# Kernel optimization log

Measured on AMD Instinct MI355X. Metric: run time of the kernel, lower is better.

The kernel has to match this reference:

```python
import jax, jax.numpy as jnp
import numpy as np


def setup_inputs() -> dict:
    key = jax.random.key(0)
    ks = jax.random.split(key, 7)
    B, N, Fin, Fout = 32, 1024, 64, 64
    s = 1.0 / np.sqrt(Fin)
    return {
        "X": jax.random.normal(ks[0], (B, N, Fin), dtype=jnp.float32),
        "A": jax.random.normal(ks[1], (B, N, N), dtype=jnp.float32),  # unused in forward, kept for signature fidelity
        "W": jax.random.uniform(ks[2], (Fin, Fout), jnp.float32, -s, s),
        "att_W": jax.random.uniform(ks[3], (Fin, Fout), jnp.float32, -s, s),
        "a": jax.random.uniform(ks[4], (Fout, Fout), jnp.float32, -s, s),
        "bias_W": jax.random.uniform(ks[5], (Fout,), jnp.float32, -s, s),
        "self_W": jax.random.uniform(ks[6], (Fin, Fout), jnp.float32, -s, s),
    }


def reference(X, A, W, att_W, a, bias_W, self_W):
    # att_X = X @ att_W : [B, N, Fout]
    att_X = jnp.einsum('bnf,fg->bng', X, att_W)
    # torch einsum 'ij,ajk->ajk' sums `a` over i => per-feature scale a.sum(0)
    scale = jnp.sum(a, axis=0)  # [Fout]
    # Z[b,i,k] = sum_j att_X[b,i,j] * scale[j] * att_X[b,k,j]  -> [B, N, N]
    Z = jnp.einsum('big,bkg->bik', att_X * scale, att_X)
    n = Z.shape[1]
    Z = Z * (1.0 - jnp.eye(n, dtype=Z.dtype))  # zero diagonal per batch
    att = jax.nn.leaky_relu(Z, negative_slope=0.01)
    # H = att @ (X W) + bias_W + X self_W
    XW = jnp.einsum('bnf,fg->bng', X, W)
    H = jnp.einsum('bnm,bmg->bng', att, XW) + bias_W
    H = H + jnp.einsum('bnf,fg->bng', X, self_W)
    return H
```

## Files before the change

kernel.cpp:

```cpp
#include <hip/hip_runtime.h>

#define DEV __device__ __forceinline__
typedef short s16x8 __attribute__((ext_vector_type(8)));
typedef float f32x16 __attribute__((ext_vector_type(16)));
typedef unsigned short u16;

#define WAIT_VMCNT(N) asm volatile("s_waitcnt vmcnt(" #N ")" ::: "memory")
#define CFENCE asm volatile("" ::: "memory")

DEV unsigned cvt_pk_bf16(float lo, float hi) {
  unsigned r;
  asm volatile("v_cvt_pk_bf16_f32 %0, %1, %2" : "=v"(r) : "v"(lo), "v"(hi));
  return r;
}
DEV u16 f2bf(float f) {
  unsigned u = __builtin_bit_cast(unsigned, f);
  unsigned r = u + 0x7fffu + ((u >> 16) & 1u);
  return (u16)(r >> 16);
}
DEV float bf2f(u16 u) { return __builtin_bit_cast(float, (unsigned)u << 16); }
DEV f32x16 zero16() {
  f32x16 v;
  #pragma unroll
  for (int i = 0; i < 16; ++i) v[i] = 0.f;
  return v;
}

DEV void gld16(const u16* g, u16* l) {
  __builtin_amdgcn_global_load_lds(
      (const __attribute__((address_space(1))) void*)g,
      (__attribute__((address_space(3))) void*)l, 16, 0, 0);
}

DEV void stage_tile64(const u16* __restrict__ gbase, size_t stride, u16* lbuf, int t) {
  #pragma unroll
  for (int p = 0; p < 2; ++p) {
    int c = p * 256 + t;
    int row = c >> 3, s = c & 7;
    int gck = s ^ (row & 7);
    const u16* src = gbase + (size_t)row * stride + gck * 8;
    u16* dst = lbuf + (size_t)(p * 256 + (t & 192)) * 8;
    gld16(src, dst);
  }
}

DEV s16x8 frag(const u16* buf, int row, int chunk) {
  return *(const s16x8*)(buf + row * 64 + ((chunk ^ (row & 7)) << 3));
}

DEV int kswz(int row, int d) {
  return row * 64 + ((((d >> 3) ^ (row & 7)) << 3) | (d & 7));
}

DEV void stage_wt(const float* __restrict__ src, u16* dst, int t) {
  #pragma unroll
  for (int r = 0; r < 4; ++r) {
    int e = (r * 256 + t) * 4;
    int f = e >> 6, g0 = e & 63;
    float4 v = *(const float4*)(src + f * 64 + g0);
    float vv[4] = {v.x, v.y, v.z, v.w};
    #pragma unroll
    for (int j = 0; j < 4; ++j) {
      int g = g0 + j;
      dst[g * 64 + ((((f >> 3) ^ (g & 7)) << 3) | (f & 7))] = f2bf(vv[j]);
    }
  }
}

__global__ __launch_bounds__(256) void prep_kernel(
    const float* __restrict__ X, const float* __restrict__ W,
    const float* __restrict__ attW, const float* __restrict__ Aa,
    const float* __restrict__ biasW, const float* __restrict__ selfW,
    u16* __restrict__ Kbf, u16* __restrict__ Vt, u16* __restrict__ Bb,
    float* __restrict__ scal_ws) {
  __shared__ __align__(16) u16 Xl[64 * 64];
  __shared__ __align__(16) u16 Wt[3][64 * 64];
  __shared__ __align__(16) u16 Bl[64 * 64];
  __shared__ __align__(16) u16 Vl[64 * 72];
  __shared__ float sc4[4][64];

  const int t = threadIdx.x;
  const int b = blockIdx.x;
  const int n0 = blockIdx.y * 64;
  const int r0 = b * 1024 + n0;
  const bool sblk = (blockIdx.x == 0 && blockIdx.y == 0);
  const int lane = t & 63, w = t >> 6, h = lane >> 5, ln = lane & 31;
  const int rg = (w >> 1) * 32;
  const int cf = w & 1;
  const int d = cf * 32 + ln;

  if (sblk) {
    int qt = t >> 6, dd = t & 63;
    float s = 0.f;
    #pragma unroll
    for (int i = 0; i < 16; ++i) s += Aa[(qt * 16 + i) * 64 + dd];
    sc4[qt][dd] = s;
  }

  #pragma unroll
  for (int p = 0; p < 2; ++p) {
    int c = p * 256 + t;
    int row = c >> 3, ck = c & 7;
    const float4* src = (const float4*)(X + (size_t)(r0 + row) * 64 + ck * 8);
    float4 a0 = src[0], a1 = src[1];
    unsigned* dst = (unsigned*)&Xl[row * 64 + ((ck ^ (row & 7)) << 3)];
    dst[0] = cvt_pk_bf16(a0.x, a0.y);
    dst[1] = cvt_pk_bf16(a0.z, a0.w);
    dst[2] = cvt_pk_bf16(a1.x, a1.y);
    dst[3] = cvt_pk_bf16(a1.z, a1.w);
  }
  stage_wt(attW, &Wt[0][0], t);
  stage_wt(W, &Wt[1][0], t);
  stage_wt(selfW, &Wt[2][0], t);
  __syncthreads();

  s16x8 xa[4];
  #pragma unroll
  for (int ks = 0; ks < 4; ++ks) xa[ks] = frag(Xl, rg + ln, ks * 2 + h);

  f32x16 aA = zero16(), aW = zero16(), aS = zero16();
  #pragma unroll
  for (int ks = 0; ks < 4; ++ks) {
    s16x8 bA = frag(&Wt[0][0], d, ks * 2 + h);
    s16x8 bW = frag(&Wt[1][0], d, ks * 2 + h);
    s16x8 bS = frag(&Wt[2][0], d, ks * 2 + h);
    aA = __builtin_amdgcn_mfma_f32_32x32x16_bf16(xa[ks], bA, aA, 0, 0, 0);
    aW = __builtin_amdgcn_mfma_f32_32x32x16_bf16(xa[ks], bW, aW, 0, 0, 0);
    aS = __builtin_amdgcn_mfma_f32_32x32x16_bf16(xa[ks], bS, aS, 0, 0, 0);
  }
  __syncthreads();

  const float bi = biasW[d];
  #pragma unroll
  for (int reg = 0; reg < 16; ++reg) {
    int rl = (reg & 3) + 8 * (reg >> 2) + 4 * h;
    int row = rg + rl;
    Xl[kswz(row, d)] = f2bf(aA[reg]);
    Bl[kswz(row, d)] = f2bf(aS[reg] + bi);
  }
  #pragma unroll
  for (int pg = 0; pg < 4; ++pg) {
    int n = rg + pg * 8 + 4 * h;
    *(unsigned*)&Vl[d * 72 + n] = cvt_pk_bf16(aW[pg * 4 + 0], aW[pg * 4 + 1]);
    *(unsigned*)&Vl[d * 72 + n + 2] = cvt_pk_bf16(aW[pg * 4 + 2], aW[pg * 4 + 3]);
  }
  __syncthreads();

  #pragma unroll
  for (int p = 0; p < 2; ++p) {
    int c = p * 256 + t;
    int row = c >> 3, ck = c & 7;
    size_t go = (size_t)(r0 + row) * 64 + ck * 8;
    int lo = row * 64 + ((ck ^ (row & 7)) << 3);
    *(s16x8*)&Kbf[go] = *(const s16x8*)&Xl[lo];
    *(s16x8*)&Bb[go] = *(const s16x8*)&Bl[lo];
  }
  #pragma unroll
  for (int p = 0; p < 2; ++p) {
    int c = p * 256 + t;
    int dd = c >> 3, ck = c & 7;
    *(s16x8*)&Vt[(size_t)(b * 64 + dd) * 1024 + n0 + ck * 8] =
        *(const s16x8*)&Vl[dd * 72 + ck * 8];
  }
  if (sblk && t < 64)
    scal_ws[t] = sc4[0][t] + sc4[1][t] + sc4[2][t] + sc4[3][t];
}

#define PROC(SV, DG, PWV)                                                      \
  do {                                                                         \
    float p_[16];                                                              \
    _Pragma("unroll") for (int r_ = 0; r_ < 16; ++r_) {                        \
      float v_ = (SV)[r_];                                                     \
      p_[r_] = fmaxf(v_, 0.f) + 0.01f * fminf(v_, 0.f);                        \
    }                                                                          \
    if (DG) {                                                                  \
      _Pragma("unroll") for (int r_ = 0; r_ < 16; ++r_) {                      \
        int rl_ = (r_ & 3) + 8 * (r_ >> 2) + 4 * h;                            \
        p_[r_] = (rl_ == ln) ? 0.f : p_[r_];                                   \
      }                                                                        \
    }                                                                          \
    unsigned pk_[8];                                                           \
    _Pragma("unroll") for (int i_ = 0; i_ < 8; ++i_)                           \
        pk_[i_] = cvt_pk_bf16(p_[2 * i_], p_[2 * i_ + 1]);                     \
    auto a0_ = __builtin_amdgcn_permlane32_swap(pk_[0], pk_[2], false, false); \
    auto a1_ = __builtin_amdgcn_permlane32_swap(pk_[1], pk_[3], false, false); \
    auto a2_ = __builtin_amdgcn_permlane32_swap(pk_[4], pk_[6], false, false); \
    auto a3_ = __builtin_amdgcn_permlane32_swap(pk_[5], pk_[7], false, false); \
    PWV[0][0] = a0_[0]; PWV[0][1] = a1_[0]; PWV[0][2] = a0_[1];                \
    PWV[0][3] = a1_[1]; PWV[1][0] = a2_[0]; PWV[1][1] = a3_[0];                \
    PWV[1][2] = a2_[1]; PWV[1][3] = a3_[1];                                    \
  } while (0)

__global__ __launch_bounds__(256) void attn_kernel(
    const u16* __restrict__ Kbf, const u16* __restrict__ Vt,
    const u16* __restrict__ Bb, const float* __restrict__ scal_ws,
    float* __restrict__ Hout) {
  __shared__ __align__(16) u16 ring[4][2][4096];

  const int t = threadIdx.x;
  const int b = blockIdx.x;
  const int qt = blockIdx.y;
  const int q0 = qt * 128;
  const int lane = t & 63, w = t >> 6, h = lane >> 5, ln = lane & 31;
  const int qb = q0 + w * 32;
  const int start = ((qt << 1) + (b >> 3)) & 15;

  const u16* Kg = Kbf + (size_t)b * 65536;
  const u16* Vg = Vt + (size_t)b * 65536;

  #pragma unroll
  for (int i = 0; i < 3; ++i) {
    int tt = (start + i) & 15;
    stage_tile64(Kg + (size_t)tt * 64 * 64, 64, &ring[i][0][0], t);
    stage_tile64(Vg + tt * 64, 1024, &ring[i][1][0], t);
  }

  s16x8 qf[4];
  #pragma unroll
  for (int ks = 0; ks < 4; ++ks) {
    s16x8 raw = *(const s16x8*)(Kg + (size_t)(qb + ln) * 64 + ks * 16 + h * 8);
    float4 sA = *(const float4*)(scal_ws + ks * 16 + h * 8);
    float4 sB = *(const float4*)(scal_ws + ks * 16 + h * 8 + 4);
    union { unsigned u[4]; s16x8 v; } qq;
    qq.u[0] = cvt_pk_bf16(bf2f((u16)raw[0]) * sA.x, bf2f((u16)raw[1]) * sA.y);
    qq.u[1] = cvt_pk_bf16(bf2f((u16)raw[2]) * sA.z, bf2f((u16)raw[3]) * sA.w);
    qq.u[2] = cvt_pk_bf16(bf2f((u16)raw[4]) * sB.x, bf2f((u16)raw[5]) * sB.y);
    qq.u[3] = cvt_pk_bf16(bf2f((u16)raw[6]) * sB.z, bf2f((u16)raw[7]) * sB.w);
    qf[ks] = qq.v;
  }

  f32x16 o0 = zero16(), o1 = zero16();

  #pragma unroll 1
  for (int i = 0; i < 16; ++i) {
    const int tt = (start + i) & 15;
    const int kv0 = tt * 64;
    if (i <= 13) {
      WAIT_VMCNT(8);
    } else if (i == 14) {
      WAIT_VMCNT(4);
    } else {
      WAIT_VMCNT(0);
    }
    __builtin_amdgcn_s_barrier();
    CFENCE;
    if (i < 13) {
      const int nt_ = (start + i + 3) & 15;
      const int ns = (i + 3) & 3;
      stage_tile64(Kg + (size_t)nt_ * 64 * 64, 64, &ring[ns][0][0], t);
      stage_tile64(Vg + nt_ * 64, 1024, &ring[ns][1][0], t);
    }
    const u16* Kl = &ring[i & 3][0][0];
    const u16* Vl = &ring[i & 3][1][0];

    f32x16 s0 = zero16(), s1 = zero16();
    __builtin_amdgcn_s_setprio(1);
    #pragma unroll
    for (int ks = 0; ks < 4; ++ks) {
      s0 = __builtin_amdgcn_mfma_f32_32x32x16_bf16(frag(Kl, ln, ks * 2 + h), qf[ks], s0, 0, 0, 0);
      s1 = __builtin_amdgcn_mfma_f32_32x32x16_bf16(frag(Kl, 32 + ln, ks * 2 + h), qf[ks], s1, 0, 0, 0);
    }
    __builtin_amdgcn_s_setprio(0);

    const bool dg0 = (kv0 == qb);
    const bool dg1 = (kv0 + 32 == qb);
    unsigned pw0[2][4], pw1[2][4];
    PROC(s0, dg0, pw0);
    PROC(s1, dg1, pw1);

    __builtin_amdgcn_s_setprio(1);
    #pragma unroll
    for (int c = 0; c < 4; ++c) {
      union { unsigned u[4]; s16x8 v; } pb;
      pb.u[0] = (c < 2 ? pw0 : pw1)[c & 1][0];
      pb.u[1] = (c < 2 ? pw0 : pw1)[c & 1][1];
      pb.u[2] = (c < 2 ? pw0 : pw1)[c & 1][2];
      pb.u[3] = (c < 2 ? pw0 : pw1)[c & 1][3];
      o0 = __builtin_amdgcn_mfma_f32_32x32x16_bf16(frag(Vl, ln, c * 2 + h), pb.v, o0, 0, 0, 0);
      o1 = __builtin_amdgcn_mfma_f32_32x32x16_bf16(frag(Vl, 32 + ln, c * 2 + h), pb.v, o1, 0, 0, 0);
    }
    __builtin_amdgcn_s_setprio(0);
  }

  __syncthreads();

  float* Ow = (float*)&ring[0][0][0] + (size_t)w * 2048;
  #pragma unroll
  for (int reg = 0; reg < 16; ++reg) {
    int rl = (reg & 3) + 8 * (reg >> 2) + 4 * h;
    int d0 = rl, d1 = 32 + rl;
    Ow[ln * 64 + ((((d0 >> 2) ^ (ln & 15)) << 2) | (d0 & 3))] = o0[reg];
    Ow[ln * 64 + ((((d1 >> 2) ^ (ln & 15)) << 2) | (d1 & 3))] = o1[reg];
  }
  #pragma unroll
  for (int p = 0; p < 8; ++p) {
    int row = p * 4 + (lane >> 4);
    int g = lane & 15;
    int off = row * 64 + ((g ^ (row & 15)) << 2);
    float4 v = *(const float4*)&Ow[off];
    size_t go = ((size_t)b * 1024 + qb + row) * 64 + g * 4;
    const short4 bv = *(const short4*)(Bb + go);
    v.x += bf2f((u16)bv.x);
    v.y += bf2f((u16)bv.y);
    v.z += bf2f((u16)bv.z);
    v.w += bf2f((u16)bv.w);
    *(float4*)(Hout + go) = v;
  }
}

extern "C" void kernel_launch(void* const* d_in, const int* in_sizes, int n_in,
                              void* d_out, int out_size, void* d_ws, size_t ws_size,
                              hipStream_t stream) {
  const float* X = (const float*)d_in[0];
  const float* W = (const float*)d_in[2];
  const float* attW = (const float*)d_in[3];
  const float* a = (const float*)d_in[4];
  const float* biasW = (const float*)d_in[5];
  const float* selfW = (const float*)d_in[6];
  float* H = (float*)d_out;

  u16* Kbf = (u16*)d_ws;
  u16* Vt = Kbf + (size_t)32 * 1024 * 64;
  u16* Bb = Vt + (size_t)32 * 1024 * 64;
  float* scal = (float*)(Bb + (size_t)32 * 1024 * 64);

  prep_kernel<<<dim3(32, 16), 256, 0, stream>>>(X, W, attW, a, biasW, selfW,
                                                Kbf, Vt, Bb, scal);
  attn_kernel<<<dim3(32, 8), 256, 0, stream>>>(Kbf, Vt, Bb, scal, H);
}
```

Baseline: 34.33 us.

## Split KV tile across warps with 64-query groups and cross-warp output reduction

Restructures the attention kernel's warp work split. Each warp now handles 64 queries and half of each 64-key tile, instead of 32 queries and the full tile. K fragments stay in registers and are prefetched for the next tile, and V fragments are loaded once per tile and reused across two query halves. The two key-half partial outputs are summed through shared memory in the epilogue. Other changes: the rotated tile start order is dropped, and leaky ReLU becomes a single max. The new layout costs more accumulator registers and extra epilogue barriers.

```diff
diff --git a/kernel.cpp b/kernel.cpp
--- a/kernel.cpp
+++ b/kernel.cpp
@@ -171,7 +171,7 @@
     float p_[16];                                                              \
     _Pragma("unroll") for (int r_ = 0; r_ < 16; ++r_) {                        \
       float v_ = (SV)[r_];                                                     \
-      p_[r_] = fmaxf(v_, 0.f) + 0.01f * fminf(v_, 0.f);                        \
+      p_[r_] = fmaxf(v_, 0.01f * v_);                                          \
     }                                                                          \
     if (DG) {                                                                  \
       _Pragma("unroll") for (int r_ = 0; r_ < 16; ++r_) {                      \
@@ -199,45 +199,67 @@
 
   const int t = threadIdx.x;
   const int b = blockIdx.x;
-  const int qt = blockIdx.y;
-  const int q0 = qt * 128;
+  const int q0 = blockIdx.y * 128;
   const int lane = t & 63, w = t >> 6, h = lane >> 5, ln = lane & 31;
-  const int qb = q0 + w * 32;
-  const int start = ((qt << 1) + (b >> 3)) & 15;
+  const int qg = w & 1;
+  const int kvh = w >> 1;
 
   const u16* Kg = Kbf + (size_t)b * 65536;
   const u16* Vg = Vt + (size_t)b * 65536;
 
+  s16x8 qraw[2][4];
+  #pragma unroll
+  for (int qh = 0; qh < 2; ++qh)
+    #pragma unroll
+    for (int ks = 0; ks < 4; ++ks)
+      qraw[qh][ks] = *(const s16x8*)(
+          Kg + (size_t)(q0 + qg * 64 + qh * 32 + ln) * 64 + ks * 16 + h * 8);
+  float4 sA[4], sB[4];
+  #pragma unroll
+  for (int ks = 0; ks < 4; ++ks) {
+    sA[ks] = *(const float4*)(scal_ws + ks * 16 + h * 8);
+    sB[ks] = *(const float4*)(scal_ws + ks * 16 + h * 8 + 4);
+  }
+
   #pragma unroll
   for (int i = 0; i < 3; ++i) {
-    int tt = (start + i) & 15;
-    stage_tile64(Kg + (size_t)tt * 64 * 64, 64, &ring[i][0][0], t);
-    stage_tile64(Vg + tt * 64, 1024, &ring[i][1][0], t);
-  }
-
-  s16x8 qf[4];
-  #pragma unroll
-  for (int ks = 0; ks < 4; ++ks) {
-    s16x8 raw = *(const s16x8*)(Kg + (size_t)(qb + ln) * 64 + ks * 16 + h * 8);
-    float4 sA = *(const float4*)(scal_ws + ks * 16 + h * 8);
-    float4 sB = *(const float4*)(scal_ws + ks * 16 + h * 8 + 4);
-    union { unsigned u[4]; s16x8 v; } qq;
-    qq.u[0] = cvt_pk_bf16(bf2f((u16)raw[0]) * sA.x, bf2f((u16)raw[1]) * sA.y);
-    qq.u[1] = cvt_pk_bf16(bf2f((u16)raw[2]) * sA.z, bf2f((u16)raw[3]) * sA.w);
-    qq.u[2] = cvt_pk_bf16(bf2f((u16)raw[4]) * sB.x, bf2f((u16)raw[5]) * sB.y);
-    qq.u[3] = cvt_pk_bf16(bf2f((u16)raw[6]) * sB.z, bf2f((u16)raw[7]) * sB.w);
-    qf[ks] = qq.v;
-  }
-
-  f32x16 o0 = zero16(), o1 = zero16();
+    stage_tile64(Kg + (size_t)i * 4096, 64, &ring[i][0][0], t);
+    stage_tile64(Vg + i * 64, 1024, &ring[i][1][0], t);
+  }
+
+  s16x8 qf[2][4];
+  #pragma unroll
+  for (int qh = 0; qh < 2; ++qh)
+    #pragma unroll
+    for (int ks = 0; ks < 4; ++ks) {
+      union { unsigned u[4]; s16x8 v; } qq;
+      qq.u[0] = cvt_pk_bf16(bf2f((u16)qraw[qh][ks][0]) * sA[ks].x,
+                            bf2f((u16)qraw[qh][ks][1]) * sA[ks].y);
+      qq.u[1] = cvt_pk_bf16(bf2f((u16)qraw[qh][ks][2]) * sA[ks].z,
+                            bf2f((u16)qraw[qh][ks][3]) * sA[ks].w);
+      qq.u[2] = cvt_pk_bf16(bf2f((u16)qraw[qh][ks][4]) * sB[ks].x,
+                            bf2f((u16)qraw[qh][ks][5]) * sB[ks].y);
+      qq.u[3] = cvt_pk_bf16(bf2f((u16)qraw[qh][ks][6]) * sB[ks].z,
+                            bf2f((u16)qraw[qh][ks][7]) * sB[ks].w);
+      qf[qh][ks] = qq.v;
+    }
+
+  WAIT_VMCNT(8);
+  __builtin_amdgcn_s_barrier();
+  CFENCE;
+
+  s16x8 kf[4];
+  #pragma unroll
+  for (int ks = 0; ks < 4; ++ks)
+    kf[ks] = frag(&ring[0][0][0], kvh * 32 + ln, ks * 2 + h);
+
+  f32x16 o00 = zero16(), o01 = zero16();
+  f32x16 o10 = zero16(), o11 = zero16();
 
   #pragma unroll 1
   for (int i = 0; i < 16; ++i) {
-    const int tt = (start + i) & 15;
-    const int kv0 = tt * 64;
-    if (i <= 13) {
-      WAIT_VMCNT(8);
-    } else if (i == 14) {
+    const int kv0 = i * 64;
+    if (i < 14) {
       WAIT_VMCNT(4);
     } else {
       WAIT_VMCNT(0);
@@ -245,66 +267,95 @@
     __builtin_amdgcn_s_barrier();
     CFENCE;
     if (i < 13) {
-      const int nt_ = (start + i + 3) & 15;
       const int ns = (i + 3) & 3;
-      stage_tile64(Kg + (size_t)nt_ * 64 * 64, 64, &ring[ns][0][0], t);
-      stage_tile64(Vg + nt_ * 64, 1024, &ring[ns][1][0], t);
-    }
-    const u16* Kl = &ring[i & 3][0][0];
+      stage_tile64(Kg + (size_t)(i + 3) * 4096, 64, &ring[ns][0][0], t);
+      stage_tile64(Vg + (i + 3) * 64, 1024, &ring[ns][1][0], t);
+    }
     const u16* Vl = &ring[i & 3][1][0];
+
+    s16x8 vf[2][2];
+    #pragma unroll
+    for (int dh = 0; dh < 2; ++dh)
+      #pragma unroll
+      for (int c = 0; c < 2; ++c)
+        vf[dh][c] = frag(Vl, dh * 32 + ln, (kvh * 2 + c) * 2 + h);
 
     f32x16 s0 = zero16(), s1 = zero16();
     __builtin_amdgcn_s_setprio(1);
     #pragma unroll
     for (int ks = 0; ks < 4; ++ks) {
-      s0 = __builtin_amdgcn_mfma_f32_32x32x16_bf16(frag(Kl, ln, ks * 2 + h), qf[ks], s0, 0, 0, 0);
-      s1 = __builtin_amdgcn_mfma_f32_32x32x16_bf16(frag(Kl, 32 + ln, ks * 2 + h), qf[ks], s1, 0, 0, 0);
+      s0 = __builtin_amdgcn_mfma_f32_32x32x16_bf16(kf[ks], qf[0][ks], s0, 0, 0, 0);
+      s1 = __builtin_amdgcn_mfma_f32_32x32x16_bf16(kf[ks], qf[1][ks], s1, 0, 0, 0);
     }
     __builtin_amdgcn_s_setprio(0);
 
-    const bool dg0 = (kv0 == qb);
-    const bool dg1 = (kv0 + 32 == qb);
+    const bool dg0 = (kv0 + kvh * 32) == (q0 + qg * 64);
+    const bool dg1 = (kv0 + kvh * 32) == (q0 + qg * 64 + 32);
     unsigned pw0[2][4], pw1[2][4];
     PROC(s0, dg0, pw0);
     PROC(s1, dg1, pw1);
 
+    if (i < 15) {
+      const u16* Kn = &ring[(i + 1) & 3][0][0];
+      #pragma unroll
+      for (int ks = 0; ks < 4; ++ks)
+        kf[ks] = frag(Kn, kvh * 32 + ln, ks * 2 + h);
+    }
+
     __builtin_amdgcn_s_setprio(1);
     #pragma unroll
-    for (int c = 0; c < 4; ++c) {
-      union { unsigned u[4]; s16x8 v; } pb;
-      pb.u[0] = (c < 2 ? pw0 : pw1)[c & 1][0];
-      pb.u[1] = (c < 2 ? pw0 : pw1)[c & 1][1];
-      pb.u[2] = (c < 2 ? pw0 : pw1)[c & 1][2];
-      pb.u[3] = (c < 2 ? pw0 : pw1)[c & 1][3];
-      o0 = __builtin_amdgcn_mfma_f32_32x32x16_bf16(frag(Vl, ln, c * 2 + h), pb.v, o0, 0, 0, 0);
-      o1 = __builtin_amdgcn_mfma_f32_32x32x16_bf16(frag(Vl, 32 + ln, c * 2 + h), pb.v, o1, 0, 0, 0);
+    for (int c = 0; c < 2; ++c) {
+      union { unsigned u[4]; s16x8 v; } pb0, pb1;
+      #pragma unroll
+      for (int j = 0; j < 4; ++j) { pb0.u[j] = pw0[c][j]; pb1.u[j] = pw1[c][j]; }
+      o00 = __builtin_amdgcn_mfma_f32_32x32x16_bf16(vf[0][c], pb0.v, o00, 0, 0, 0);
+      o01 = __builtin_amdgcn_mfma_f32_32x32x16_bf16(vf[0][c], pb1.v, o01, 0, 0, 0);
+      o10 = __builtin_amdgcn_mfma_f32_32x32x16_bf16(vf[1][c], pb0.v, o10, 0, 0, 0);
+      o11 = __builtin_amdgcn_mfma_f32_32x32x16_bf16(vf[1][c], pb1.v, o11, 0, 0, 0);
     }
     __builtin_amdgcn_s_setprio(0);
   }
 
   __syncthreads();
 
-  float* Ow = (float*)&ring[0][0][0] + (size_t)w * 2048;
-  #pragma unroll
-  for (int reg = 0; reg < 16; ++reg) {
-    int rl = (reg & 3) + 8 * (reg >> 2) + 4 * h;
-    int d0 = rl, d1 = 32 + rl;
-    Ow[ln * 64 + ((((d0 >> 2) ^ (ln & 15)) << 2) | (d0 & 3))] = o0[reg];
-    Ow[ln * 64 + ((((d1 >> 2) ^ (ln & 15)) << 2) | (d1 & 3))] = o1[reg];
-  }
-  #pragma unroll
-  for (int p = 0; p < 8; ++p) {
-    int row = p * 4 + (lane >> 4);
-    int g = lane & 15;
-    int off = row * 64 + ((g ^ (row & 15)) << 2);
-    float4 v = *(const float4*)&Ow[off];
-    size_t go = ((size_t)b * 1024 + qb + row) * 64 + g * 4;
-    const short4 bv = *(const short4*)(Bb + go);
-    v.x += bf2f((u16)bv.x);
-    v.y += bf2f((u16)bv.y);
-    v.z += bf2f((u16)bv.z);
-    v.w += bf2f((u16)bv.w);
-    *(float4*)(Hout + go) = v;
+  float* R0 = (float*)&ring[0][0][0];
+  float* R1 = R0 + 4096;
+  #pragma unroll
+  for (int g = 0; g < 2; ++g) {
+    if (qg == g) {
+      float* Rd = kvh ? R1 : R0;
+      #pragma unroll
+      for (int qh = 0; qh < 2; ++qh) {
+        const f32x16& oA = qh ? o01 : o00;
+        const f32x16& oB = qh ? o11 : o10;
+        int q = qh * 32 + ln;
+        #pragma unroll
+        for (int reg = 0; reg < 16; ++reg) {
+          int rl = (reg & 3) + 8 * (reg >> 2) + 4 * h;
+          int d0 = rl, d1 = 32 + rl;
+          Rd[q * 64 + ((((d0 >> 2) ^ (q & 15)) << 2) | (d0 & 3))] = oA[reg];
+          Rd[q * 64 + ((((d1 >> 2) ^ (q & 15)) << 2) | (d1 & 3))] = oB[reg];
+        }
+      }
+    }
+    __syncthreads();
+    #pragma unroll
+    for (int e = 0; e < 4; ++e) {
+      int idx = e * 256 + t;
+      int q = idx >> 4, dgp = idx & 15;
+      int off = q * 64 + ((dgp ^ (q & 15)) << 2);
+      float4 v0 = *(const float4*)&R0[off];
+      float4 v1 = *(const float4*)&R1[off];
+      size_t go = ((size_t)b * 1024 + q0 + g * 64 + q) * 64 + dgp * 4;
+      const short4 bv = *(const short4*)(Bb + go);
+      float4 v;
+      v.x = v0.x + v1.x + bf2f((u16)bv.x);
+      v.y = v0.y + v1.y + bf2f((u16)bv.y);
+      v.z = v0.z + v1.z + bf2f((u16)bv.z);
+      v.w = v0.w + v1.w + bf2f((u16)bv.w);
+      *(float4*)(Hout + go) = v;
+    }
+    if (g == 0) __syncthreads();
   }
 }
 
```

New measurement: 33.99 us (median of 2 runs). No clear change (-1.0%).
